# Optimization experiments

Hardware: AMD Instinct MI355X
Metric: run time of the kernel (lower is better)

## Reference

```python
import jax, jax.numpy as jnp
import numpy as np

DIM = 256   # model dim (forced by gate Linear(32,4): d = 32 = DIM//H)
H = 8       # heads (hard-coded by mask.repeat(1,8,1,1))
D = DIM // H
B = 256     # batch
NS = 100    # skeleton tokens (sub-block size)
NQ = 64     # query tokens
N = NS + NQ # 164
NE = 4      # experts
HID = 50    # expert hidden
LN_EPS = 1e-5


def setup_inputs() -> dict:
    key = jax.random.key(0)
    ks = jax.random.split(key, 12)
    s = 0.02
    return {
        "x": jax.random.normal(ks[0], (B, N, DIM), jnp.float32),
        "mask": jax.random.randint(ks[1], (B, N), 0, 2).astype(bool),
        "w_qk_s": jax.random.normal(ks[2], (DIM, 2 * DIM), jnp.float32) * s,
        "w_qk_q": jax.random.normal(ks[3], (DIM, 2 * DIM), jnp.float32) * s,
        "w_v": jax.random.normal(ks[4], (DIM, DIM), jnp.float32) * s,
        "w_gate": jax.random.normal(ks[5], (D, NE), jnp.float32) * s,
        "b_gate": jnp.zeros((NE,), jnp.float32),
        "ln_gamma": jnp.ones((NE,), jnp.float32),
        "ln_beta": jnp.zeros((NE,), jnp.float32),
        "w1": jax.random.normal(ks[6], (NE, NS, HID), jnp.float32) * s,
        "b1": jnp.zeros((NE, HID), jnp.float32),
        "w2": jax.random.normal(ks[7], (NE, HID, NS), jnp.float32) * s,
        "b2": jnp.zeros((NE, NS), jnp.float32),
        "w_out": jax.random.normal(ks[8], (DIM, DIM), jnp.float32) * s,
        "b_out": jnp.zeros((DIM,), jnp.float32),
    }


def reference(x, mask, w_qk_s, w_qk_q, w_v, w_gate, b_gate, ln_gamma, ln_beta,
              w1, b1, w2, b2, w_out, b_out):
    b, n, dim = x.shape
    scale = dim ** -0.5  # scale_with_head=False -> dim**-0.5

    def to_heads(t):  # (b, m, H*D) -> (b, H, m, D)
        return t.reshape(b, -1, H, D).transpose(0, 2, 1, 3)

    # separate qk projections for skeleton (first 100) vs query (last 64) tokens
    q_s, k_s = jnp.split(x[:, :NS] @ w_qk_s, 2, axis=-1)
    q_q, k_q = jnp.split(x[:, NS:] @ w_qk_q, 2, axis=-1)
    q = jnp.concatenate([to_heads(q_s), to_heads(q_q)], axis=2)  # (b,H,N,D)
    k = jnp.concatenate([to_heads(k_s), to_heads(k_q)], axis=2)
    v = to_heads(x @ w_v)

    # gates: RAW reshape of x (b,n,H*D) -> (b,H,n,D) (memory reinterpretation,
    # as in torch x.reshape), detached, sliced to first 100 'rows'
    gx = jax.lax.stop_gradient(x).reshape(b, H, n, D)[:, :, :NS, :]
    g = gx @ w_gate + b_gate                              # (b,H,100,4)
    mu = g.mean(-1, keepdims=True)
    var = g.var(-1, keepdims=True)
    g = (g - mu) / jnp.sqrt(var + LN_EPS) * ln_gamma + ln_beta
    gates = jax.nn.softmax(g, axis=-1)                    # (b,H,100,4)

    dots = jnp.einsum('bhid,bhjd->bhij', q, k) * scale    # (b,H,N,N)
    mask_value = -jnp.finfo(dots.dtype).max
    dots = jnp.where(mask[:, None, None, :], mask_value, dots)

    # soft-MoE over the 100x100 sub-block (experts applied along key axis)
    attn_q = dots[:, :, :NS, :NS]                         # (b,H,100,100)
    h1 = jax.nn.relu(jnp.einsum('bhij,ejk->bheik', jax.nn.relu(attn_q), w1)
                     + b1[:, None, :])                    # (b,H,4,100,50)
    eo = jax.nn.relu(jnp.einsum('bheik,ekj->bheij', h1, w2)
                     + b2[:, None, :])                    # (b,H,4,100,100)
    moes = jnp.einsum('bheij,bhie->bhij', eo, gates)      # (b,H,100,100)

    dots = dots.at[:, :, :NS, :NS].add(moes)
    attn = jax.nn.softmax(dots, axis=-1)
    out = jnp.einsum('bhij,bhjd->bhid', attn, v)          # (b,H,N,D)
    out = out.transpose(0, 2, 1, 3).reshape(b, n, dim)
    return out @ w_out + b_out
```

## Files before the change

### kernel.cpp

```cpp
#include <hip/hip_runtime.h>

typedef __bf16 bf16x8 __attribute__((ext_vector_type(8)));
typedef __bf16 bf16x4 __attribute__((ext_vector_type(4)));
typedef float  f32x4  __attribute__((ext_vector_type(4)));

__device__ __forceinline__ bf16x8 ldb8(const __bf16* p) {
    return *reinterpret_cast<const bf16x8*>(p);
}
__device__ __forceinline__ bf16x8 zero8() {
    bf16x8 z;
    #pragma unroll
    for (int i = 0; i < 8; i++) z[i] = (__bf16)0.f;
    return z;
}
__device__ __forceinline__ __bf16 ldw(const void* p, int i, int m) {
    return m ? (__bf16)((const float*)p)[i] : ((const __bf16*)p)[i];
}
__device__ __forceinline__ bf16x8 ldx8(const void* p, size_t ei, int m) {
    if (m) {
        const float* f = (const float*)p + ei;
        f32x4 a = *reinterpret_cast<const f32x4*>(f);
        f32x4 b = *reinterpret_cast<const f32x4*>(f + 4);
        bf16x8 r;
        #pragma unroll
        for (int u = 0; u < 4; u++) { r[u] = (__bf16)a[u]; r[4 + u] = (__bf16)b[u]; }
        return r;
    }
    return ldb8((const __bf16*)p + ei);
}

__global__ __launch_bounds__(256) void detect_kernel(
    const void* x, const void* mask, int* modes, int* maskws)
{
    __shared__ int v32bad, v16bad, sbad;
    const int t = threadIdx.x, bid = blockIdx.x;
    if (t == 0) { v32bad = 0; v16bad = 0; sbad = 0; }
    __syncthreads();
    const unsigned int* mw = (const unsigned int*)mask;
    int b32 = 0, b16 = 0;
    for (int i = t; i < 10496; i += 256) {
        unsigned int w = mw[i];
        if (!(w == 0u || w == 1u || w == 0x3F800000u)) b32++;
        unsigned int h0 = w & 0xFFFFu, h1 = w >> 16;
        if (!(h0 == 0u || h0 == 1u || h0 == 0x3F80u)) b16++;
        if (!(h1 == 0u || h1 == 1u || h1 == 0x3F80u)) b16++;
    }
    if (b32) atomicAdd(&v32bad, b32);
    if (b16) atomicAdd(&v16bad, b16);
    if (bid == 0) {
        const unsigned int* xw = (const unsigned int*)x;
        int bad = 0;
        for (int i = t; i < 2048; i += 256) {
            unsigned int w = xw[i];
            unsigned int el = (w >> 7) & 0xFF, eh = (w >> 23) & 0xFF;
            if (el >= 0x94 || el == 0xFF) bad++;
            if (eh >= 0x94 || eh == 0xFF) bad++;
        }
        if (bad) atomicAdd(&sbad, bad);
    }
    __syncthreads();
    const int mmode = (v32bad == 0) ? 0 : ((v16bad == 0) ? 2 : 1);
    if (bid == 0 && t == 0) { modes[0] = (sbad > 64) ? 1 : 0; modes[1] = mmode; }
    const int lo = bid * 656, hi = lo + 656;
    for (int i = lo + t; i < hi; i += 256) {
        int val;
        if (mmode == 0)      val = (((const int*)mask)[i] != 0);
        else if (mmode == 2) val = (((const unsigned short*)mask)[i] != 0);
        else                 val = (((const unsigned char*)mask)[i] != 0);
        maskws[i] = val;
    }
}

__global__ __launch_bounds__(256) void prep_kernel(
    const void* wqks, const void* wqkq, const void* wv, const void* w1,
    const void* w2, const void* wout, const void* wg, const void* bg,
    const void* lng, const void* lnb, const void* b1, const void* b2,
    const void* bout, const int* __restrict__ modes,
    __bf16* __restrict__ Wts, __bf16* __restrict__ Wtq,
    __bf16* __restrict__ w1t, __bf16* __restrict__ w2t,
    __bf16* __restrict__ wot, __bf16* __restrict__ wsm)
{
    const int m = modes[0];
    int i = blockIdx.x * 256 + threadIdx.x;
    if (i < 196608) {
        int n = i >> 8, k = i & 255;
        __bf16 vs, vq;
        if (n < 512) { vs = ldw(wqks, k * 512 + n, m); vq = ldw(wqkq, k * 512 + n, m); }
        else         { vs = ldw(wv, k * 256 + (n - 512), m); vq = vs; }
        Wts[i] = vs; Wtq[i] = vq;
        return;
    }
    i -= 196608;
    if (i < 32768) {
        int e = i >> 13, r = i & 8191, n = r >> 7, k = r & 127;
        w1t[i] = (n < 50 && k < 100) ? ldw(w1, (e * 100 + k) * 50 + n, m) : (__bf16)0.f;
        return;
    }
    i -= 32768;
    if (i < 28672) {
        int e = i / 7168, r = i % 7168, n = r >> 6, k = r & 63;
        w2t[i] = (n < 100 && k < 50) ? ldw(w2, (e * 50 + k) * 100 + n, m) : (__bf16)0.f;
        return;
    }
    i -= 28672;
    if (i < 65536) {
        int n = i >> 8, k = i & 255;
        wot[i] = ldw(wout, k * 256 + n, m);
        return;
    }
    i -= 65536;
    if (i < 996) {
        __bf16 v;
        if (i < 128)      v = ldw(wg, i, m);
        else if (i < 132) v = ldw(bg, i - 128, m);
        else if (i < 136) v = ldw(lng, i - 132, m);
        else if (i < 140) v = ldw(lnb, i - 136, m);
        else if (i < 340) v = ldw(b1, i - 140, m);
        else if (i < 740) v = ldw(b2, i - 340, m);
        else              v = ldw(bout, i - 740, m);
        wsm[i] = v;
    }
}

__global__ __launch_bounds__(256, 2) void qkv_kernel(
    const void* __restrict__ x, const __bf16* __restrict__ Wts,
    const __bf16* __restrict__ Wtq, const __bf16* __restrict__ wsm,
    const int* __restrict__ modes,
    __bf16* __restrict__ q, __bf16* __restrict__ k, __bf16* __restrict__ v,
    float* __restrict__ gates)
{
    __shared__ __bf16 xs[32][264];
    __shared__ float wgf[128];
    __shared__ float gcst[12];
    const int m = modes[0];
    const int b = blockIdx.y;
    const int mt = blockIdx.x;
    const __bf16* Wt = (mt < 4) ? Wts : Wtq;
    const int rbase = (mt < 4) ? mt * 32 : 100 + (mt - 4) * 32;
    const int tid = threadIdx.x;

    if (tid < 128) wgf[tid] = (float)wsm[tid];
    if (tid < 12)  gcst[tid] = (float)wsm[128 + tid];
    for (int c = tid; c < 1024; c += 256) {
        int row = c >> 5, part = c & 31;
        bf16x8 val = ldx8(x, ((size_t)b * 164 + rbase + row) * 256 + part * 8, m);
        *reinterpret_cast<bf16x8*>(&xs[row][part * 8]) = val;
    }
    __syncthreads();

    {
        int jg = rbase * 8 + tid;
        int h = jg / 164;
        int j = jg - h * 164;
        if (j < 100) {
            const __bf16* xp = &xs[tid >> 3][(tid & 7) * 32];
            float g[4] = {gcst[0], gcst[1], gcst[2], gcst[3]};
            #pragma unroll
            for (int p = 0; p < 4; p++) {
                bf16x8 xv = ldb8(xp + p * 8);
                #pragma unroll
                for (int u = 0; u < 8; u++) {
                    float f = (float)xv[u];
                    #pragma unroll
                    for (int e = 0; e < 4; e++) g[e] += f * wgf[(p * 8 + u) * 4 + e];
                }
            }
            float mu = 0.25f * (g[0] + g[1] + g[2] + g[3]);
            float var = 0.25f * ((g[0]-mu)*(g[0]-mu) + (g[1]-mu)*(g[1]-mu) +
                                 (g[2]-mu)*(g[2]-mu) + (g[3]-mu)*(g[3]-mu));
            float is = rsqrtf(var + 1e-5f);
            float mx = -3.0e38f;
            #pragma unroll
            for (int e = 0; e < 4; e++) {
                g[e] = (g[e] - mu) * is * gcst[4 + e] + gcst[8 + e];
                mx = fmaxf(mx, g[e]);
            }
            float s = 0.f;
            #pragma unroll
            for (int e = 0; e < 4; e++) { g[e] = __expf(g[e] - mx); s += g[e]; }
            float inv = 1.f / s;
            float4 gv = make_float4(g[0]*inv, g[1]*inv, g[2]*inv, g[3]*inv);
            *reinterpret_cast<float4*>(&gates[((size_t)(b * 8 + h) * 100 + j) * 4]) = gv;
        }
    }

    const int w = tid >> 6, l = tid & 63, lr = l & 15, lc = l >> 4;
    f32x4 acc[2][12];
    #pragma unroll
    for (int ms = 0; ms < 2; ms++)
        #pragma unroll
        for (int nt = 0; nt < 12; nt++) acc[ms][nt] = (f32x4){0.f, 0.f, 0.f, 0.f};

    #pragma unroll
    for (int kt = 0; kt < 8; kt++) {
        bf16x8 a0 = ldb8(&xs[lr][kt * 32 + lc * 8]);
        bf16x8 a1 = ldb8(&xs[16 + lr][kt * 32 + lc * 8]);
        #pragma unroll
        for (int nt = 0; nt < 12; nt++) {
            bf16x8 bb = ldb8(Wt + (size_t)(w * 192 + nt * 16 + lr) * 256 + kt * 32 + lc * 8);
            acc[0][nt] = __builtin_amdgcn_mfma_f32_16x16x32_bf16(a0, bb, acc[0][nt], 0, 0, 0);
            acc[1][nt] = __builtin_amdgcn_mfma_f32_16x16x32_bf16(a1, bb, acc[1][nt], 0, 0, 0);
        }
    }
    #pragma unroll
    for (int ms = 0; ms < 2; ms++) {
        #pragma unroll
        for (int nt = 0; nt < 12; nt++) {
            int c = w * 192 + nt * 16 + lr;
            __bf16* dst; int ch;
            if (c < 256)      { dst = q; ch = c; }
            else if (c < 512) { dst = k; ch = c - 256; }
            else              { dst = v; ch = c - 512; }
            int hh = ch >> 5, d = ch & 31;
            #pragma unroll
            for (int r = 0; r < 4; r++) {
                int i = rbase + ms * 16 + lc * 4 + r;
                if (mt >= 4 || i < 100)
                    dst[(((size_t)b * 8 + hh) * 164 + i) * 32 + d] = (__bf16)acc[ms][nt][r];
            }
        }
    }
}

__global__ __launch_bounds__(256, 4) void attn_kernel(
    const __bf16* __restrict__ qg, const __bf16* __restrict__ kg,
    const __bf16* __restrict__ vg, const float* __restrict__ gatesg,
    const int* __restrict__ maskg, const __bf16* __restrict__ w1t,
    const __bf16* __restrict__ w2t, const __bf16* __restrict__ wsm,
    __bf16* __restrict__ ohg)
{
    __shared__ __align__(16) __bf16 lds[20352];
    const int RS_OFF = 7040;
    const int H1_OFF = 15744;
    const int P_OFF  = 7040;

    const __bf16* b1g = wsm + 140;
    const __bf16* b2g = wsm + 340;
    const int bh = blockIdx.x, rt = blockIdx.y, b = bh >> 3, tid = threadIdx.x;
    const int w = tid >> 6, l = tid & 63, lr = l & 15, lc = l >> 4;
    const int m0 = w * 16;

    const __bf16* kbase = kg + (size_t)bh * 164 * 32;
    for (int c = tid; c < 704; c += 256) {
        int row = c >> 2, part = c & 3;
        bf16x8 val = (row < 164) ? ldb8(kbase + row * 32 + part * 8) : zero8();
        *reinterpret_cast<bf16x8*>(&lds[row * 40 + part * 8]) = val;
    }
    unsigned mbits = 0;
    #pragma unroll
    for (int nt = 0; nt < 11; nt++) {
        int j = nt * 16 + lr;
        int bad = (j < 164) ? maskg[b * 164 + j] : 1;
        mbits |= (bad ? 1u : 0u) << nt;
    }
    __syncthreads();

    int qrow = rt * 64 + m0 + lr; if (qrow > 163) qrow = 163;
    bf16x8 afq = ldb8(qg + ((size_t)bh * 164 + qrow) * 32 + lc * 8);
    f32x4 raw[12];
    #pragma unroll
    for (int nt = 0; nt < 11; nt++) {
        bf16x8 bf = ldb8(&lds[(nt * 16 + lr) * 40 + lc * 8]);
        f32x4 acc = {0.f, 0.f, 0.f, 0.f};
        acc = __builtin_amdgcn_mfma_f32_16x16x32_bf16(afq, bf, acc, 0, 0, 0);
        bool bad = (mbits >> nt) & 1;
        #pragma unroll
        for (int r = 0; r < 4; r++)
            raw[nt][r] = bad ? -1e30f : acc[r] * 0.0625f;
    }
    #pragma unroll
    for (int r = 0; r < 4; r++) raw[11][r] = -1e30f;

    #pragma unroll
    for (int nt = 0; nt < 8; nt++) {
        int j = nt * 16 + lr;
        #pragma unroll
        for (int r = 0; r < 4; r++) {
            float v = raw[nt][r];
            v = (j >= 100 || v < 0.f) ? 0.f : v;
            lds[RS_OFF + (m0 + lc * 4 + r) * 136 + j] = (__bf16)v;
        }
    }
    __syncthreads();

    const __bf16* vbase = vg + (size_t)bh * 164 * 32;
    {
        int dd = tid & 31;
        #pragma unroll
        for (int p = 0; p < 3; p++) {
            int jg = (tid >> 5) + p * 8;
            int j0 = jg * 8;
            bf16x8 vv = zero8();
            if (j0 < 164) {
                #pragma unroll
                for (int u = 0; u < 8; u++)
                    if (j0 + u < 164) vv[u] = vbase[(size_t)(j0 + u) * 32 + dd];
            }
            *reinterpret_cast<bf16x8*>(&lds[dd * 200 + j0]) = vv;
        }
    }

    if (rt < 2) {
        const int gi0 = rt * 64 + m0 + lc * 4;
        for (int e = 0; e < 4; e++) {
            bf16x8 sa[4];
            #pragma unroll
            for (int kt = 0; kt < 4; kt++)
                sa[kt] = ldb8(&lds[RS_OFF + (m0 + lr) * 136 + kt * 32 + lc * 8]);
            #pragma unroll
            for (int nt = 0; nt < 4; nt++) {
                f32x4 acc = {0.f, 0.f, 0.f, 0.f};
                #pragma unroll
                for (int kt = 0; kt < 4; kt++) {
                    bf16x8 bb = ldb8(w1t + (size_t)(e * 64 + nt * 16 + lr) * 128 + kt * 32 + lc * 8);
                    acc = __builtin_amdgcn_mfma_f32_16x16x32_bf16(sa[kt], bb, acc, 0, 0, 0);
                }
                int n = nt * 16 + lr;
                float bias = (n < 50) ? (float)b1g[e * 50 + n] : 0.f;
                #pragma unroll
                for (int r = 0; r < 4; r++) {
                    float v = acc[r] + bias;
                    if (v < 0.f) v = 0.f;
                    lds[H1_OFF + (m0 + lc * 4 + r) * 72 + n] = (__bf16)v;
                }
            }
            bf16x8 ha0 = ldb8(&lds[H1_OFF + (m0 + lr) * 72 + lc * 8]);
            bf16x8 ha1 = ldb8(&lds[H1_OFF + (m0 + lr) * 72 + 32 + lc * 8]);
            float gt[4];
            #pragma unroll
            for (int r = 0; r < 4; r++) {
                int gi = gi0 + r;
                gt[r] = (gi < 100) ? gatesg[((size_t)bh * 100 + gi) * 4 + e] : 0.f;
            }
            #pragma unroll
            for (int nt = 0; nt < 7; nt++) {
                f32x4 acc = {0.f, 0.f, 0.f, 0.f};
                bf16x8 bb0 = ldb8(w2t + (size_t)(e * 112 + nt * 16 + lr) * 64 + lc * 8);
                acc = __builtin_amdgcn_mfma_f32_16x16x32_bf16(ha0, bb0, acc, 0, 0, 0);
                bf16x8 bb1 = ldb8(w2t + (size_t)(e * 112 + nt * 16 + lr) * 64 + 32 + lc * 8);
                acc = __builtin_amdgcn_mfma_f32_16x16x32_bf16(ha1, bb1, acc, 0, 0, 0);
                int n = nt * 16 + lr;
                float bias = (n < 100) ? (float)b2g[e * 100 + n] : 0.f;
                #pragma unroll
                for (int r = 0; r < 4; r++) {
                    float v = acc[r] + bias;
                    if (v < 0.f) v = 0.f;
                    raw[nt][r] += v * gt[r];
                }
            }
        }
    }
    __syncthreads();

    #pragma unroll
    for (int r = 0; r < 4; r++) {
        float m2 = -3.0e38f;
        #pragma unroll
        for (int nt = 0; nt < 12; nt++) m2 = fmaxf(m2, raw[nt][r]);
        m2 = fmaxf(m2, __shfl_xor(m2, 1, 64));
        m2 = fmaxf(m2, __shfl_xor(m2, 2, 64));
        m2 = fmaxf(m2, __shfl_xor(m2, 4, 64));
        m2 = fmaxf(m2, __shfl_xor(m2, 8, 64));
        float s2 = 0.f;
        #pragma unroll
        for (int nt = 0; nt < 12; nt++) {
            float ev = __expf(raw[nt][r] - m2);
            raw[nt][r] = ev;
            s2 += ev;
        }
        s2 += __shfl_xor(s2, 1, 64);
        s2 += __shfl_xor(s2, 2, 64);
        s2 += __shfl_xor(s2, 4, 64);
        s2 += __shfl_xor(s2, 8, 64);
        float inv = (s2 > 0.f) ? 1.f / s2 : 0.f;
        #pragma unroll
        for (int nt = 0; nt < 12; nt++)
            lds[P_OFF + (m0 + lc * 4 + r) * 200 + nt * 16 + lr] = (__bf16)(raw[nt][r] * inv);
    }
    __syncthreads();

    int gi = rt * 64 + m0 + lr;
    #pragma unroll
    for (int nt = 0; nt < 2; nt++) {
        f32x4 acc = {0.f, 0.f, 0.f, 0.f};
        #pragma unroll
        for (int kt = 0; kt < 6; kt++) {
            bf16x8 va = ldb8(&lds[(nt * 16 + lr) * 200 + kt * 32 + lc * 8]);
            bf16x8 pb = ldb8(&lds[P_OFF + (m0 + lr) * 200 + kt * 32 + lc * 8]);
            acc = __builtin_amdgcn_mfma_f32_16x16x32_bf16(va, pb, acc, 0, 0, 0);
        }
        if (gi < 164) {
            bf16x4 ov;
            #pragma unroll
            for (int r = 0; r < 4; r++) ov[r] = (__bf16)acc[r];
            *reinterpret_cast<bf16x4*>(&ohg[((size_t)bh * 164 + gi) * 32 + nt * 16 + lc * 4]) = ov;
        }
    }
}

__global__ __launch_bounds__(256) void outproj_kernel(
    const __bf16* __restrict__ oh, const __bf16* __restrict__ wot,
    const __bf16* __restrict__ wsm, float* __restrict__ out)
{
    const __bf16* bout = wsm + 740;
    const int b = blockIdx.y;
    const int mt = blockIdx.x >> 1;
    const int ntile = blockIdx.x & 1;
    const int tid = threadIdx.x;
    const int w = tid >> 6, l = tid & 63, lr = l & 15, lc = l >> 4;
    int row = mt * 64 + w * 16 + lr; if (row > 163) row = 163;
    f32x4 acc[8];
    #pragma unroll
    for (int nt = 0; nt < 8; nt++) acc[nt] = (f32x4){0.f, 0.f, 0.f, 0.f};
    #pragma unroll
    for (int kt = 0; kt < 8; kt++) {
        bf16x8 a = ldb8(oh + (((size_t)b * 8 + kt) * 164 + row) * 32 + lc * 8);
        #pragma unroll
        for (int nt = 0; nt < 8; nt++) {
            bf16x8 bb = ldb8(wot + (size_t)(ntile * 128 + nt * 16 + lr) * 256 + kt * 32 + lc * 8);
            acc[nt] = __builtin_amdgcn_mfma_f32_16x16x32_bf16(a, bb, acc[nt], 0, 0, 0);
        }
    }
    #pragma unroll
    for (int nt = 0; nt < 8; nt++) {
        int n = ntile * 128 + nt * 16 + lr;
        float bias = (float)bout[n];
        #pragma unroll
        for (int r = 0; r < 4; r++) {
            int i = mt * 64 + w * 16 + lc * 4 + r;
            if (i < 164)
                out[((size_t)b * 164 + i) * 256 + n] = acc[nt][r] + bias;
        }
    }
}

extern "C" void kernel_launch(void* const* d_in, const int* in_sizes, int n_in,
                              void* d_out, int out_size, void* d_ws, size_t ws_size,
                              hipStream_t stream) {
    const void* x      = d_in[0];
    const void* mask   = d_in[1];
    const void* w_qk_s = d_in[2];
    const void* w_qk_q = d_in[3];
    const void* w_v    = d_in[4];
    const void* w_gate = d_in[5];
    const void* b_gate = d_in[6];
    const void* ln_g   = d_in[7];
    const void* ln_b   = d_in[8];
    const void* w1     = d_in[9];
    const void* b1     = d_in[10];
    const void* w2     = d_in[11];
    const void* b2     = d_in[12];
    const void* w_out  = d_in[13];
    const void* b_out  = d_in[14];
    float* out = (float*)d_out;

    char* ws = (char*)d_ws;
    size_t off = 0;
    auto nextp = [&](size_t bytes) {
        char* p = ws + off;
        off += (bytes + 255) & ~(size_t)255;
        return p;
    };
    const size_t QKV_ELEMS = (size_t)256 * 8 * 164 * 32;
    int*    modes  = (int*)nextp(64);
    int*    maskws = (int*)nextp((size_t)41984 * 4);
    __bf16* qws  = (__bf16*)nextp(QKV_ELEMS * 2);
    __bf16* kws  = (__bf16*)nextp(QKV_ELEMS * 2);
    __bf16* vws  = (__bf16*)nextp(QKV_ELEMS * 2);
    __bf16* ohws = (__bf16*)nextp(QKV_ELEMS * 2);
    float*  gws  = (float*)nextp((size_t)2048 * 100 * 4 * 4);
    __bf16* Wts  = (__bf16*)nextp(768 * 256 * 2);
    __bf16* Wtq  = (__bf16*)nextp(768 * 256 * 2);
    __bf16* w1t  = (__bf16*)nextp(4 * 64 * 128 * 2);
    __bf16* w2t  = (__bf16*)nextp(4 * 112 * 64 * 2);
    __bf16* wot  = (__bf16*)nextp(256 * 256 * 2);
    __bf16* wsm  = (__bf16*)nextp(996 * 2);

    detect_kernel<<<64, 256, 0, stream>>>(x, mask, modes, maskws);
    prep_kernel<<<1268, 256, 0, stream>>>(w_qk_s, w_qk_q, w_v, w1, w2, w_out,
                                          w_gate, b_gate, ln_g, ln_b, b1, b2,
                                          b_out, modes, Wts, Wtq, w1t, w2t, wot, wsm);
    qkv_kernel<<<dim3(6, 256), 256, 0, stream>>>(x, Wts, Wtq, wsm, modes,
                                                 qws, kws, vws, gws);
    attn_kernel<<<dim3(2048, 3), 256, 0, stream>>>(qws, kws, vws, gws, maskws,
                                                   w1t, w2t, wsm, ohws);
    outproj_kernel<<<dim3(6, 256), 256, 0, stream>>>(ohws, wot, wsm, out);
}
```

Before: 553.4 us.

## Store V transposed, split QKV/outproj tiles, double-buffer MoE hidden LDS, prefetch V

The QKV kernel now writes V in a transposed, padded layout (d-major, 176 stride), so the attention kernel loads it with vector loads instead of scalar strided gathers. The V loads are issued before the softmax and stored to LDS afterward, which overlaps their latency. QKV and out-projection grids are doubled by splitting output columns, lowering register use per block. In the MoE loop, gates are loaded once as float4, the score A-fragments are hoisted out of the expert loop, and the hidden buffer alternates between two LDS regions. Non-MoE row tiles also skip writing the score block.

```diff
diff --git a/kernel.cpp b/kernel.cpp
--- a/kernel.cpp
+++ b/kernel.cpp
@@ -126,7 +126,7 @@
     const void* __restrict__ x, const __bf16* __restrict__ Wts,
     const __bf16* __restrict__ Wtq, const __bf16* __restrict__ wsm,
     const int* __restrict__ modes,
-    __bf16* __restrict__ q, __bf16* __restrict__ k, __bf16* __restrict__ v,
+    __bf16* __restrict__ q, __bf16* __restrict__ k, __bf16* __restrict__ vt,
     float* __restrict__ gates)
 {
     __shared__ __bf16 xs[32][264];
@@ -134,7 +134,8 @@
     __shared__ float gcst[12];
     const int m = modes[0];
     const int b = blockIdx.y;
-    const int mt = blockIdx.x;
+    const int mt = blockIdx.x >> 1;
+    const int half = blockIdx.x & 1;
     const __bf16* Wt = (mt < 4) ? Wts : Wtq;
     const int rbase = (mt < 4) ? mt * 32 : 100 + (mt - 4) * 32;
     const int tid = threadIdx.x;
@@ -148,7 +149,7 @@
     }
     __syncthreads();
 
-    {
+    if (half == 0) {
         int jg = rbase * 8 + tid;
         int h = jg / 164;
         int j = jg - h * 164;
@@ -185,19 +186,19 @@
     }
 
     const int w = tid >> 6, l = tid & 63, lr = l & 15, lc = l >> 4;
-    f32x4 acc[2][12];
+    f32x4 acc[2][6];
     #pragma unroll
     for (int ms = 0; ms < 2; ms++)
         #pragma unroll
-        for (int nt = 0; nt < 12; nt++) acc[ms][nt] = (f32x4){0.f, 0.f, 0.f, 0.f};
+        for (int nt = 0; nt < 6; nt++) acc[ms][nt] = (f32x4){0.f, 0.f, 0.f, 0.f};
 
     #pragma unroll
     for (int kt = 0; kt < 8; kt++) {
         bf16x8 a0 = ldb8(&xs[lr][kt * 32 + lc * 8]);
         bf16x8 a1 = ldb8(&xs[16 + lr][kt * 32 + lc * 8]);
         #pragma unroll
-        for (int nt = 0; nt < 12; nt++) {
-            bf16x8 bb = ldb8(Wt + (size_t)(w * 192 + nt * 16 + lr) * 256 + kt * 32 + lc * 8);
+        for (int nt = 0; nt < 6; nt++) {
+            bf16x8 bb = ldb8(Wt + (size_t)(half * 384 + w * 96 + nt * 16 + lr) * 256 + kt * 32 + lc * 8);
             acc[0][nt] = __builtin_amdgcn_mfma_f32_16x16x32_bf16(a0, bb, acc[0][nt], 0, 0, 0);
             acc[1][nt] = __builtin_amdgcn_mfma_f32_16x16x32_bf16(a1, bb, acc[1][nt], 0, 0, 0);
         }
@@ -205,18 +206,28 @@
     #pragma unroll
     for (int ms = 0; ms < 2; ms++) {
         #pragma unroll
-        for (int nt = 0; nt < 12; nt++) {
-            int c = w * 192 + nt * 16 + lr;
-            __bf16* dst; int ch;
-            if (c < 256)      { dst = q; ch = c; }
-            else if (c < 512) { dst = k; ch = c - 256; }
-            else              { dst = v; ch = c - 512; }
-            int hh = ch >> 5, d = ch & 31;
-            #pragma unroll
-            for (int r = 0; r < 4; r++) {
-                int i = rbase + ms * 16 + lc * 4 + r;
-                if (mt >= 4 || i < 100)
-                    dst[(((size_t)b * 8 + hh) * 164 + i) * 32 + d] = (__bf16)acc[ms][nt][r];
+        for (int nt = 0; nt < 6; nt++) {
+            int c = half * 384 + w * 96 + nt * 16 + lr;
+            int i0 = rbase + ms * 16 + lc * 4;
+            if (c < 512) {
+                __bf16* dst; int ch;
+                if (c < 256) { dst = q; ch = c; }
+                else         { dst = k; ch = c - 256; }
+                int hh = ch >> 5, d = ch & 31;
+                #pragma unroll
+                for (int r = 0; r < 4; r++) {
+                    int i = i0 + r;
+                    if (mt >= 4 || i < 100)
+                        dst[(((size_t)b * 8 + hh) * 164 + i) * 32 + d] = (__bf16)acc[ms][nt][r];
+                }
+            } else {
+                int ch = c - 512, hh = ch >> 5, d = ch & 31;
+                if (mt >= 4 || i0 < 100) {
+                    bf16x4 pv;
+                    #pragma unroll
+                    for (int r = 0; r < 4; r++) pv[r] = (__bf16)acc[ms][nt][r];
+                    *reinterpret_cast<bf16x4*>(&vt[((size_t)(b * 8 + hh) * 32 + d) * 176 + i0]) = pv;
+                }
             }
         }
     }
@@ -224,14 +235,13 @@
 
 __global__ __launch_bounds__(256, 4) void attn_kernel(
     const __bf16* __restrict__ qg, const __bf16* __restrict__ kg,
-    const __bf16* __restrict__ vg, const float* __restrict__ gatesg,
+    const __bf16* __restrict__ vtg, const float* __restrict__ gatesg,
     const int* __restrict__ maskg, const __bf16* __restrict__ w1t,
     const __bf16* __restrict__ w2t, const __bf16* __restrict__ wsm,
     __bf16* __restrict__ ohg)
 {
     __shared__ __align__(16) __bf16 lds[20352];
     const int RS_OFF = 7040;
-    const int H1_OFF = 15744;
     const int P_OFF  = 7040;
 
     const __bf16* b1g = wsm + 140;
@@ -253,10 +263,10 @@
         int bad = (j < 164) ? maskg[b * 164 + j] : 1;
         mbits |= (bad ? 1u : 0u) << nt;
     }
-    __syncthreads();
-
     int qrow = rt * 64 + m0 + lr; if (qrow > 163) qrow = 163;
     bf16x8 afq = ldb8(qg + ((size_t)bh * 164 + qrow) * 32 + lc * 8);
+    __syncthreads();
+
     f32x4 raw[12];
     #pragma unroll
     for (int nt = 0; nt < 11; nt++) {
@@ -271,42 +281,37 @@
     #pragma unroll
     for (int r = 0; r < 4; r++) raw[11][r] = -1e30f;
 
-    #pragma unroll
-    for (int nt = 0; nt < 8; nt++) {
-        int j = nt * 16 + lr;
-        #pragma unroll
-        for (int r = 0; r < 4; r++) {
-            float v = raw[nt][r];
-            v = (j >= 100 || v < 0.f) ? 0.f : v;
-            lds[RS_OFF + (m0 + lc * 4 + r) * 136 + j] = (__bf16)v;
-        }
-    }
-    __syncthreads();
-
-    const __bf16* vbase = vg + (size_t)bh * 164 * 32;
-    {
-        int dd = tid & 31;
-        #pragma unroll
-        for (int p = 0; p < 3; p++) {
-            int jg = (tid >> 5) + p * 8;
-            int j0 = jg * 8;
-            bf16x8 vv = zero8();
-            if (j0 < 164) {
-                #pragma unroll
-                for (int u = 0; u < 8; u++)
-                    if (j0 + u < 164) vv[u] = vbase[(size_t)(j0 + u) * 32 + dd];
+    if (rt < 2) {
+        #pragma unroll
+        for (int nt = 0; nt < 8; nt++) {
+            int j = nt * 16 + lr;
+            #pragma unroll
+            for (int r = 0; r < 4; r++) {
+                float v = raw[nt][r];
+                v = (j >= 100 || v < 0.f) ? 0.f : v;
+                lds[RS_OFF + (m0 + lc * 4 + r) * 136 + j] = (__bf16)v;
             }
-            *reinterpret_cast<bf16x8*>(&lds[dd * 200 + j0]) = vv;
-        }
-    }
+        }
+    }
+    __syncthreads();
 
     if (rt < 2) {
         const int gi0 = rt * 64 + m0 + lc * 4;
+        float4 gv[4];
+        #pragma unroll
+        for (int r = 0; r < 4; r++) {
+            int gi = gi0 + r;
+            gv[r] = (gi < 100)
+                ? *reinterpret_cast<const float4*>(&gatesg[((size_t)bh * 100 + gi) * 4])
+                : make_float4(0.f, 0.f, 0.f, 0.f);
+        }
+        bf16x8 sa[4];
+        #pragma unroll
+        for (int kt = 0; kt < 4; kt++)
+            sa[kt] = ldb8(&lds[RS_OFF + (m0 + lr) * 136 + kt * 32 + lc * 8]);
+        #pragma unroll
         for (int e = 0; e < 4; e++) {
-            bf16x8 sa[4];
-            #pragma unroll
-            for (int kt = 0; kt < 4; kt++)
-                sa[kt] = ldb8(&lds[RS_OFF + (m0 + lr) * 136 + kt * 32 + lc * 8]);
+            const int HO = (e & 1) ? 15744 : 0;
             #pragma unroll
             for (int nt = 0; nt < 4; nt++) {
                 f32x4 acc = {0.f, 0.f, 0.f, 0.f};
@@ -321,17 +326,11 @@
                 for (int r = 0; r < 4; r++) {
                     float v = acc[r] + bias;
                     if (v < 0.f) v = 0.f;
-                    lds[H1_OFF + (m0 + lc * 4 + r) * 72 + n] = (__bf16)v;
+                    lds[HO + (m0 + lc * 4 + r) * 72 + n] = (__bf16)v;
                 }
             }
-            bf16x8 ha0 = ldb8(&lds[H1_OFF + (m0 + lr) * 72 + lc * 8]);
-            bf16x8 ha1 = ldb8(&lds[H1_OFF + (m0 + lr) * 72 + 32 + lc * 8]);
-            float gt[4];
-            #pragma unroll
-            for (int r = 0; r < 4; r++) {
-                int gi = gi0 + r;
-                gt[r] = (gi < 100) ? gatesg[((size_t)bh * 100 + gi) * 4 + e] : 0.f;
-            }
+            bf16x8 ha0 = ldb8(&lds[HO + (m0 + lr) * 72 + lc * 8]);
+            bf16x8 ha1 = ldb8(&lds[HO + (m0 + lr) * 72 + 32 + lc * 8]);
             #pragma unroll
             for (int nt = 0; nt < 7; nt++) {
                 f32x4 acc = {0.f, 0.f, 0.f, 0.f};
@@ -345,29 +344,65 @@
                 for (int r = 0; r < 4; r++) {
                     float v = acc[r] + bias;
                     if (v < 0.f) v = 0.f;
-                    raw[nt][r] += v * gt[r];
+                    float ge = (e == 0) ? gv[r].x : (e == 1) ? gv[r].y
+                             : (e == 2) ? gv[r].z : gv[r].w;
+                    raw[nt][r] += v * ge;
                 }
             }
         }
     }
     __syncthreads();
 
+    const __bf16* vtb = vtg + (size_t)bh * 32 * 176;
+    int off0, off1, off2;
+    bf16x8 vv0, vv1, vv2;
+    {
+        int c = tid;
+        int row = c / 22, j0 = (c - row * 22) * 8;
+        off0 = row * 200 + j0;
+        if (j0 < 168) {
+            vv0 = ldb8(vtb + row * 176 + j0);
+            if (j0 == 160) { vv0[4] = (__bf16)0.f; vv0[5] = (__bf16)0.f; vv0[6] = (__bf16)0.f; vv0[7] = (__bf16)0.f; }
+        } else vv0 = zero8();
+    }
+    {
+        int c = tid + 256;
+        int row = c / 22, j0 = (c - row * 22) * 8;
+        off1 = row * 200 + j0;
+        if (j0 < 168) {
+            vv1 = ldb8(vtb + row * 176 + j0);
+            if (j0 == 160) { vv1[4] = (__bf16)0.f; vv1[5] = (__bf16)0.f; vv1[6] = (__bf16)0.f; vv1[7] = (__bf16)0.f; }
+        } else vv1 = zero8();
+    }
+    if (tid < 192) {
+        int c = tid + 512;
+        int row = c / 22, j0 = (c - row * 22) * 8;
+        off2 = row * 200 + j0;
+        if (j0 < 168) {
+            vv2 = ldb8(vtb + row * 176 + j0);
+            if (j0 == 160) { vv2[4] = (__bf16)0.f; vv2[5] = (__bf16)0.f; vv2[6] = (__bf16)0.f; vv2[7] = (__bf16)0.f; }
+        } else vv2 = zero8();
+    }
+
     #pragma unroll
     for (int r = 0; r < 4; r++) {
-        float m2 = -3.0e38f;
-        #pragma unroll
-        for (int nt = 0; nt < 12; nt++) m2 = fmaxf(m2, raw[nt][r]);
+        float x0 = fmaxf(raw[0][r], raw[1][r]);
+        float x1 = fmaxf(raw[2][r], raw[3][r]);
+        float x2 = fmaxf(raw[4][r], raw[5][r]);
+        float x3 = fmaxf(raw[6][r], raw[7][r]);
+        float x4 = fmaxf(raw[8][r], raw[9][r]);
+        float x5 = fmaxf(raw[10][r], raw[11][r]);
+        float m2 = fmaxf(fmaxf(fmaxf(x0, x1), fmaxf(x2, x3)), fmaxf(x4, x5));
         m2 = fmaxf(m2, __shfl_xor(m2, 1, 64));
         m2 = fmaxf(m2, __shfl_xor(m2, 2, 64));
         m2 = fmaxf(m2, __shfl_xor(m2, 4, 64));
         m2 = fmaxf(m2, __shfl_xor(m2, 8, 64));
-        float s2 = 0.f;
-        #pragma unroll
-        for (int nt = 0; nt < 12; nt++) {
-            float ev = __expf(raw[nt][r] - m2);
-            raw[nt][r] = ev;
-            s2 += ev;
-        }
+        #pragma unroll
+        for (int nt = 0; nt < 12; nt++) raw[nt][r] = __expf(raw[nt][r] - m2);
+        float s0 = (raw[0][r] + raw[1][r]) + (raw[2][r] + raw[3][r]);
+        float s1 = (raw[4][r] + raw[5][r]) + (raw[6][r] + raw[7][r]);
+        float s2t = (raw[8][r] + raw[9][r]) + (raw[10][r] + raw[11][r]);
+        float s2 = (s0 + s1) + s2t;
         s2 += __shfl_xor(s2, 1, 64);
         s2 += __shfl_xor(s2, 2, 64);
         s2 += __shfl_xor(s2, 4, 64);
@@ -377,6 +412,10 @@
         for (int nt = 0; nt < 12; nt++)
             lds[P_OFF + (m0 + lc * 4 + r) * 200 + nt * 16 + lr] = (__bf16)(raw[nt][r] * inv);
     }
+
+    *reinterpret_cast<bf16x8*>(&lds[off0]) = vv0;
+    *reinterpret_cast<bf16x8*>(&lds[off1]) = vv1;
+    if (tid < 192) *reinterpret_cast<bf16x8*>(&lds[off2]) = vv2;
     __syncthreads();
 
     int gi = rt * 64 + m0 + lr;
@@ -404,26 +443,26 @@
 {
     const __bf16* bout = wsm + 740;
     const int b = blockIdx.y;
-    const int mt = blockIdx.x >> 1;
-    const int ntile = blockIdx.x & 1;
+    const int mt = blockIdx.x >> 2;
+    const int ntile = blockIdx.x & 3;
     const int tid = threadIdx.x;
     const int w = tid >> 6, l = tid & 63, lr = l & 15, lc = l >> 4;
     int row = mt * 64 + w * 16 + lr; if (row > 163) row = 163;
-    f32x4 acc[8];
-    #pragma unroll
-    for (int nt = 0; nt < 8; nt++) acc[nt] = (f32x4){0.f, 0.f, 0.f, 0.f};
+    f32x4 acc[4];
+    #pragma unroll
+    for (int nt = 0; nt < 4; nt++) acc[nt] = (f32x4){0.f, 0.f, 0.f, 0.f};
     #pragma unroll
     for (int kt = 0; kt < 8; kt++) {
         bf16x8 a = ldb8(oh + (((size_t)b * 8 + kt) * 164 + row) * 32 + lc * 8);
         #pragma unroll
-        for (int nt = 0; nt < 8; nt++) {
-            bf16x8 bb = ldb8(wot + (size_t)(ntile * 128 + nt * 16 + lr) * 256 + kt * 32 + lc * 8);
+        for (int nt = 0; nt < 4; nt++) {
+            bf16x8 bb = ldb8(wot + (size_t)(ntile * 64 + nt * 16 + lr) * 256 + kt * 32 + lc * 8);
             acc[nt] = __builtin_amdgcn_mfma_f32_16x16x32_bf16(a, bb, acc[nt], 0, 0, 0);
         }
     }
     #pragma unroll
-    for (int nt = 0; nt < 8; nt++) {
-        int n = ntile * 128 + nt * 16 + lr;
+    for (int nt = 0; nt < 4; nt++) {
+        int n = ntile * 64 + nt * 16 + lr;
         float bias = (float)bout[n];
         #pragma unroll
         for (int r = 0; r < 4; r++) {
@@ -462,11 +501,12 @@
         return p;
     };
     const size_t QKV_ELEMS = (size_t)256 * 8 * 164 * 32;
+    const size_t VT_ELEMS  = (size_t)256 * 8 * 32 * 176;
     int*    modes  = (int*)nextp(64);
     int*    maskws = (int*)nextp((size_t)41984 * 4);
     __bf16* qws  = (__bf16*)nextp(QKV_ELEMS * 2);
     __bf16* kws  = (__bf16*)nextp(QKV_ELEMS * 2);
-    __bf16* vws  = (__bf16*)nextp(QKV_ELEMS * 2);
+    __bf16* vtws = (__bf16*)nextp(VT_ELEMS * 2);
     __bf16* ohws = (__bf16*)nextp(QKV_ELEMS * 2);
     float*  gws  = (float*)nextp((size_t)2048 * 100 * 4 * 4);
     __bf16* Wts  = (__bf16*)nextp(768 * 256 * 2);
@@ -480,9 +520,9 @@
     prep_kernel<<<1268, 256, 0, stream>>>(w_qk_s, w_qk_q, w_v, w1, w2, w_out,
                                           w_gate, b_gate, ln_g, ln_b, b1, b2,
                                           b_out, modes, Wts, Wtq, w1t, w2t, wot, wsm);
-    qkv_kernel<<<dim3(6, 256), 256, 0, stream>>>(x, Wts, Wtq, wsm, modes,
-                                                 qws, kws, vws, gws);
-    attn_kernel<<<dim3(2048, 3), 256, 0, stream>>>(qws, kws, vws, gws, maskws,
+    qkv_kernel<<<dim3(12, 256), 256, 0, stream>>>(x, Wts, Wtq, wsm, modes,
+                                                  qws, kws, vtws, gws);
+    attn_kernel<<<dim3(2048, 3), 256, 0, stream>>>(qws, kws, vtws, gws, maskws,
                                                    w1t, w2t, wsm, ohws);
-    outproj_kernel<<<dim3(6, 256), 256, 0, stream>>>(ohws, wot, wsm, out);
-}
+    outproj_kernel<<<dim3(12, 256), 256, 0, stream>>>(ohws, wot, wsm, out);
+}
```

After: 592.8 us. 7.1% more time.
